# Performance work log

Hardware: AMD Instinct MI355X
Metric: run time of the kernel (lower is better)

The kernel has to match this reference:

```python
import jax, jax.numpy as jnp
import numpy as np

EMBED = 1024
HEADS = 16
HEAD_DIM = EMBED // HEADS
FFN = 4096
BSZ = 2
CHUNK = 128
NCHUNK = 16
REG_LEN = CHUNK * NCHUNK   # 2048
SUM_LEN = NCHUNK           # 1 summary token per chunk
NEG = -1e9


def _layer_norm(x, g, b, eps=1e-5):
    mu = x.mean(-1, keepdims=True)
    var = ((x - mu) ** 2).mean(-1, keepdims=True)
    return (x - mu) * jax.lax.rsqrt(var + eps) * g + b


def _build_mask(reg_chunk_ranges, sum_len, reg_len):
    # True = attention allowed. Museformer hierarchical scheme:
    #   rr: reg token attends reg tokens of its OWN chunk, causally
    #   rs: reg token attends summary tokens of STRICTLY EARLIER chunks
    #   sr: summary token of chunk c attends reg tokens of chunk c
    #   ss: causal among summary tokens
    bsz = reg_chunk_ranges.shape[0]
    starts = reg_chunk_ranges[:, :, 0]                       # [B, C]
    t = jnp.arange(reg_len)
    chunk_id = (t[None, :, None] >= starts[:, None, :]).sum(-1) - 1   # [B, R]
    sum_chunk = jnp.arange(sum_len)                          # [S]
    rr = (chunk_id[:, :, None] == chunk_id[:, None, :]) & (t[None, :, None] >= t[None, None, :])
    rs = sum_chunk[None, None, :] < chunk_id[:, :, None]     # [B, R, S]
    sr = chunk_id[:, None, :] == sum_chunk[None, :, None]    # [B, S, R]
    ss = jnp.broadcast_to(sum_chunk[:, None] >= sum_chunk[None, :], (bsz, sum_len, sum_len))
    top = jnp.concatenate([ss, sr], axis=2)
    bot = jnp.concatenate([rs, rr], axis=2)
    return jnp.concatenate([top, bot], axis=1)               # [B, S+R, S+R]


def _forward(x, w_q, w_k, w_v, w_o,
             ln_sa_sum_g, ln_sa_sum_b, ln_sa_reg_g, ln_sa_reg_b,
             sum_fc1_w, sum_fc1_b, sum_fc2_w, sum_fc2_b,
             reg_fc1_w, reg_fc1_b, reg_fc2_w, reg_fc2_b,
             ln_f_sum_g, ln_f_sum_b, ln_f_reg_g, ln_f_reg_b,
             reg_chunk_ranges, sum_len, reg_len):
    bsz, total, d = x.shape
    # --- self-attention block (pre-norm, separate LN for sum/reg parts) ---
    hs = _layer_norm(x[:, :sum_len], ln_sa_sum_g, ln_sa_sum_b)
    hr = _layer_norm(x[:, sum_len:], ln_sa_reg_g, ln_sa_reg_b)
    h = jnp.concatenate([hs, hr], axis=1)
    q = (h @ w_q.T).reshape(bsz, total, HEADS, HEAD_DIM)
    k = (h @ w_k.T).reshape(bsz, total, HEADS, HEAD_DIM)
    v = (h @ w_v.T).reshape(bsz, total, HEADS, HEAD_DIM)
    scores = jnp.einsum('bqhd,bkhd->bhqk', q, k) * (HEAD_DIM ** -0.5)
    mask = _build_mask(reg_chunk_ranges, sum_len, reg_len)   # [B, T, T] bool
    scores = jnp.where(mask[:, None], scores, NEG)
    attn = jax.nn.softmax(scores, axis=-1)
    ctx = jnp.einsum('bhqk,bkhd->bqhd', attn, v).reshape(bsz, total, d)
    x = x + ctx @ w_o.T
    # --- FFN block (pre-norm, separate LN/FFN for sum/reg parts) ---
    fs = _layer_norm(x[:, :sum_len], ln_f_sum_g, ln_f_sum_b)
    fs = jax.nn.relu(fs @ sum_fc1_w.T + sum_fc1_b) @ sum_fc2_w.T + sum_fc2_b
    fr = _layer_norm(x[:, sum_len:], ln_f_reg_g, ln_f_reg_b)
    fr = jax.nn.relu(fr @ reg_fc1_w.T + reg_fc1_b) @ reg_fc2_w.T + reg_fc2_b
    return x + jnp.concatenate([fs, fr], axis=1)


def setup_inputs() -> dict:
    key = jax.random.key(0)
    ks = jax.random.split(key, 12)
    s = 0.02
    total = SUM_LEN + REG_LEN
    starts = (np.arange(NCHUNK) * CHUNK).astype(np.int32)
    ranges = np.stack([starts, starts + CHUNK], axis=-1)     # [C, 2]
    reg_chunk_ranges = jnp.asarray(np.broadcast_to(ranges, (BSZ, NCHUNK, 2)).copy())
    d = dict(
        x=jax.random.normal(ks[0], (BSZ, total, EMBED), jnp.float32),
        w_q=jax.random.normal(ks[1], (EMBED, EMBED), jnp.float32) * s,
        w_k=jax.random.normal(ks[2], (EMBED, EMBED), jnp.float32) * s,
        w_v=jax.random.normal(ks[3], (EMBED, EMBED), jnp.float32) * s,
        w_o=jax.random.normal(ks[4], (EMBED, EMBED), jnp.float32) * s,
        ln_sa_sum_g=jnp.ones((EMBED,)), ln_sa_sum_b=jnp.zeros((EMBED,)),
        ln_sa_reg_g=jnp.ones((EMBED,)), ln_sa_reg_b=jnp.zeros((EMBED,)),
        sum_fc1_w=jax.random.normal(ks[5], (FFN, EMBED), jnp.float32) * s,
        sum_fc1_b=jnp.zeros((FFN,)),
        sum_fc2_w=jax.random.normal(ks[6], (EMBED, FFN), jnp.float32) * s,
        sum_fc2_b=jnp.zeros((EMBED,)),
        reg_fc1_w=jax.random.normal(ks[7], (FFN, EMBED), jnp.float32) * s,
        reg_fc1_b=jnp.zeros((FFN,)),
        reg_fc2_w=jax.random.normal(ks[8], (EMBED, FFN), jnp.float32) * s,
        reg_fc2_b=jnp.zeros((EMBED,)),
        ln_f_sum_g=jnp.ones((EMBED,)), ln_f_sum_b=jnp.zeros((EMBED,)),
        ln_f_reg_g=jnp.ones((EMBED,)), ln_f_reg_b=jnp.zeros((EMBED,)),
        reg_chunk_ranges=reg_chunk_ranges,
        sum_len=SUM_LEN,
        reg_len=REG_LEN,
    )
    return d


def reference(x, w_q, w_k, w_v, w_o,
              ln_sa_sum_g, ln_sa_sum_b, ln_sa_reg_g, ln_sa_reg_b,
              sum_fc1_w, sum_fc1_b, sum_fc2_w, sum_fc2_b,
              reg_fc1_w, reg_fc1_b, reg_fc2_w, reg_fc2_b,
              ln_f_sum_g, ln_f_sum_b, ln_f_reg_g, ln_f_reg_b,
              reg_chunk_ranges, sum_len, reg_len):
    return _forward(x, w_q, w_k, w_v, w_o,
                    ln_sa_sum_g, ln_sa_sum_b, ln_sa_reg_g, ln_sa_reg_b,
                    sum_fc1_w, sum_fc1_b, sum_fc2_w, sum_fc2_b,
                    reg_fc1_w, reg_fc1_b, reg_fc2_w, reg_fc2_b,
                    ln_f_sum_g, ln_f_sum_b, ln_f_reg_g, ln_f_reg_b,
                    reg_chunk_ranges, sum_len, reg_len)
```

## Files before the change

kernel.cpp:

```cpp
#include <hip/hip_runtime.h>
#include <stdint.h>

typedef __attribute__((ext_vector_type(8))) short short8;
typedef __attribute__((ext_vector_type(4))) float f32x4;

__device__ __forceinline__ float bf2f(short s) {
    union { unsigned u; float f; } c;
    c.u = ((unsigned)(unsigned short)s) << 16;
    return c.f;
}
__device__ __forceinline__ short f2bf(float f) {
    union { float f; unsigned u; } c; c.f = f;
    unsigned u = c.u + 0x7fffu + ((c.u >> 16) & 1u);
    return (short)(u >> 16);
}
__device__ __forceinline__ void gll16(const short* g, short* l) {
    __builtin_amdgcn_global_load_lds(
        (const __attribute__((address_space(1))) unsigned int*)g,
        (__attribute__((address_space(3))) unsigned int*)l, 16, 0, 0);
}

__global__ __launch_bounds__(256) void cvt_w(
    const float* __restrict__ wq, const float* __restrict__ wk,
    const float* __restrict__ wv, const float* __restrict__ wo,
    const float* __restrict__ f1s, const float* __restrict__ f2s,
    const float* __restrict__ f1r, const float* __restrict__ f2r,
    short* __restrict__ dst)
{
    size_t i = ((size_t)blockIdx.x * 256 + threadIdx.x) * 4;
    const float* src; size_t off;
    if (i < 4194304) {
        int seg = (int)(i >> 20);
        src = seg == 0 ? wq : seg == 1 ? wk : seg == 2 ? wv : wo;
        off = i & 1048575;
    } else {
        size_t ii = i - 4194304;
        int seg = (int)(ii >> 22);
        src = seg == 0 ? f1s : seg == 1 ? f2s : seg == 2 ? f1r : f2r;
        off = ii & 4194303;
    }
    float4 v = *(const float4*)(src + off);
    short4 o;
    o.x = f2bf(v.x); o.y = f2bf(v.y); o.z = f2bf(v.z); o.w = f2bf(v.w);
    *(short4*)(dst + i) = o;
}

template<int PHASE>
__global__ __launch_bounds__(256) void ln_k(
    const float* __restrict__ xin, const float* __restrict__ P, float* __restrict__ x1out,
    const float* __restrict__ g_sum, const float* __restrict__ b_sum,
    const float* __restrict__ g_reg, const float* __restrict__ b_reg,
    short* __restrict__ out_all, short* __restrict__ out_s, short* __restrict__ out_r)
{
    int row = blockIdx.x;
    int b = row / 2064, t = row - b * 2064;
    int tid = threadIdx.x;
    int c = tid * 4;
    size_t base = (size_t)row * 1024 + c;
    float4 v = *(const float4*)(xin + base);
    if (PHASE == 1) {
        float4 p0 = *(const float4*)(P + base);
        float4 p1 = *(const float4*)(P + base + 4227072);
        v.x += p0.x + p1.x; v.y += p0.y + p1.y;
        v.z += p0.z + p1.z; v.w += p0.w + p1.w;
        *(float4*)(x1out + base) = v;
    }
    float s = v.x + v.y + v.z + v.w;
#pragma unroll
    for (int off = 1; off < 64; off <<= 1) s += __shfl_xor(s, off);
    __shared__ float red[8];
    if ((tid & 63) == 0) red[tid >> 6] = s;
    __syncthreads();
    float mu = (red[0] + red[1] + red[2] + red[3]) * (1.0f / 1024.0f);
    float a0 = v.x - mu, a1 = v.y - mu, a2 = v.z - mu, a3 = v.w - mu;
    float qq = a0 * a0 + a1 * a1 + a2 * a2 + a3 * a3;
#pragma unroll
    for (int off = 1; off < 64; off <<= 1) qq += __shfl_xor(qq, off);
    if ((tid & 63) == 0) red[4 + (tid >> 6)] = qq;
    __syncthreads();
    float var = (red[4] + red[5] + red[6] + red[7]) * (1.0f / 1024.0f);
    float rs = rsqrtf(var + 1e-5f);
    const float* g  = (t < 16) ? g_sum : g_reg;
    const float* be = (t < 16) ? b_sum : b_reg;
    short4 o;
    o.x = f2bf(a0 * rs * g[c]     + be[c]);
    o.y = f2bf(a1 * rs * g[c + 1] + be[c + 1]);
    o.z = f2bf(a2 * rs * g[c + 2] + be[c + 2]);
    o.w = f2bf(a3 * rs * g[c + 3] + be[c + 3]);
    short* dst;
    if (PHASE == 0) dst = out_all + (size_t)row * 1024;
    else dst = (t < 16) ? (out_s + ((size_t)b * 16 + t) * 1024)
                        : (out_r + ((size_t)b * 2048 + (t - 16)) * 1024);
    *(short4*)(dst + c) = o;
}

template<int MODE>
__global__ __launch_bounds__(256) void gemm_bt(
    const short* __restrict__ A, int M, int K, int klen,
    const short* __restrict__ B0, const short* __restrict__ B1, const short* __restrict__ B2,
    const float* __restrict__ bias,
    void* __restrict__ o0, void* __restrict__ o1, void* __restrict__ o2, int seg)
{
    const int tid = threadIdx.x;
    const int w = tid >> 6, l = tid & 63;
    const int lr = l & 15, lh = l >> 4;
    const int m0 = blockIdx.x * 128;
    int ntile = blockIdx.y, nsel = 0;
    const short* B = B0;
    if (MODE == 0) { nsel = ntile >> 3; ntile &= 7; B = nsel == 0 ? B0 : (nsel == 1 ? B1 : B2); }
    const int n0 = ntile * 128;
    const int wr = (w >> 1) * 64, wc = (w & 1) * 64;
    const int kbase = blockIdx.z * klen;

    __shared__ __align__(16) short As[3 * 4096];
    __shared__ __align__(16) short Bs[3 * 4096];

    const int srow = w * 32 + (l >> 2);
    const int scol = (((l & 3) ^ ((l >> 3) & 3))) * 8;
    int ar0 = m0 + srow;      if (ar0 > M - 1) ar0 = M - 1;
    int ar1 = m0 + srow + 16; if (ar1 > M - 1) ar1 = M - 1;
    const short* ga0 = A + (size_t)ar0 * K + scol + kbase;
    const short* ga1 = A + (size_t)ar1 * K + scol + kbase;
    const short* gb0 = B + (size_t)(n0 + srow) * K + scol + kbase;
    const short* gb1 = B + (size_t)(n0 + srow + 16) * K + scol + kbase;
    const int lofs = (w * 32) * 32;

    const int cbrd = (lh ^ ((lr >> 1) & 3)) * 8;

    f32x4 acc[4][4];
#pragma unroll
    for (int m = 0; m < 4; ++m)
#pragma unroll
        for (int n = 0; n < 4; ++n) acc[m][n] = (f32x4){0.f, 0.f, 0.f, 0.f};

    auto STAGE = [&](int j, int s) {
        const int k0 = j * 32;
        short* a = As + s * 4096 + lofs;
        short* b = Bs + s * 4096 + lofs;
        gll16(ga0 + k0, a);
        gll16(ga1 + k0, a + 512);
        gll16(gb0 + k0, b);
        gll16(gb1 + k0, b + 512);
    };

    const int nk = klen >> 5;
    STAGE(0, 0);
    STAGE(1, 1);

    int sc = 0;
    for (int t = 0; t < nk; ++t) {
        if (t < nk - 1) asm volatile("s_waitcnt vmcnt(4)" ::: "memory");
        else            asm volatile("s_waitcnt vmcnt(0)" ::: "memory");
        __builtin_amdgcn_s_barrier();
        if (t + 2 < nk) {
            int sp = sc == 0 ? 2 : sc - 1;
            STAGE(t + 2, sp);
        }
        const int cur = sc * 4096;
        short8 af[4], bfr[4];
#pragma unroll
        for (int m = 0; m < 4; ++m)
            af[m] = *(const short8*)(As + cur + (wr + m * 16 + lr) * 32 + cbrd);
#pragma unroll
        for (int n = 0; n < 4; ++n)
            bfr[n] = *(const short8*)(Bs + cur + (wc + n * 16 + lr) * 32 + cbrd);
#pragma unroll
        for (int m = 0; m < 4; ++m)
#pragma unroll
            for (int n = 0; n < 4; ++n)
                acc[m][n] = __builtin_amdgcn_mfma_f32_16x16x32_bf16(af[m], bfr[n], acc[m][n], 0, 0, 0);
        sc = sc == 2 ? 0 : sc + 1;
    }

#pragma unroll
    for (int m = 0; m < 4; ++m) {
#pragma unroll
        for (int n = 0; n < 4; ++n) {
            int gc = n0 + wc + n * 16 + lr;
#pragma unroll
            for (int j = 0; j < 4; ++j) {
                int gr = m0 + wr + m * 16 + lh * 4 + j;
                if (gr >= M) continue;
                float val = acc[m][n][j];
                if (MODE == 0) {
                    short* o = (short*)(nsel == 0 ? o0 : (nsel == 1 ? o1 : o2));
                    o[(size_t)gr * 1024 + gc] = f2bf(val);
                } else if (MODE == 1) {
                    float* P = (float*)o0 + (size_t)blockIdx.z * (size_t)seg;
                    P[(size_t)gr * 1024 + gc] = val;
                } else {
                    val += bias[gc];
                    val = val > 0.f ? val : 0.f;
                    ((short*)o0)[(size_t)gr * 4096 + gc] = f2bf(val);
                }
            }
        }
    }
}

__global__ __launch_bounds__(256) void reduce_f2reg(
    const float* __restrict__ x1, const float* __restrict__ P,
    const float* __restrict__ bias, float* __restrict__ out)
{
    size_t i = ((size_t)blockIdx.x * 256 + threadIdx.x) * 4;
    int gr = (int)(i >> 10), c = (int)(i & 1023);
    size_t g = (size_t)((gr >> 11) * 2064 + 16 + (gr & 2047)) * 1024 + c;
    float4 p0 = *(const float4*)(P + i);
    float4 p1 = *(const float4*)(P + i + 4194304);
    float4 r  = *(const float4*)(x1 + g);
    float4 bb = *(const float4*)(bias + c);
    float4 o;
    o.x = r.x + p0.x + p1.x + bb.x; o.y = r.y + p0.y + p1.y + bb.y;
    o.z = r.z + p0.z + p1.z + bb.z; o.w = r.w + p0.w + p1.w + bb.w;
    *(float4*)(out + g) = o;
}

__global__ __launch_bounds__(256) void reduce_f2sum(
    const float* __restrict__ x1, const float* __restrict__ P,
    const float* __restrict__ bias, float* __restrict__ out)
{
    int i = (blockIdx.x * 256 + threadIdx.x) * 4;
    int gr = i >> 10, c = i & 1023;
    size_t g = (size_t)((gr >> 4) * 2064 + (gr & 15)) * 1024 + c;
    float4 r  = *(const float4*)(x1 + g);
    float4 bb = *(const float4*)(bias + c);
    float ox = r.x + bb.x, oy = r.y + bb.y, oz = r.z + bb.z, ow = r.w + bb.w;
#pragma unroll
    for (int s = 0; s < 16; ++s) {
        float4 p = *(const float4*)(P + s * 32768 + i);
        ox += p.x; oy += p.y; oz += p.z; ow += p.w;
    }
    float4 o; o.x = ox; o.y = oy; o.z = oz; o.w = ow;
    *(float4*)(out + g) = o;
}

__global__ __launch_bounds__(256) void attn_reg(
    const short* __restrict__ q, const short* __restrict__ k,
    const short* __restrict__ v, short* __restrict__ ctx)
{
    __shared__ __align__(16) short Pl[128 * 168];
    __shared__ __align__(16) short Vt[64 * 168];
    short* Kl = Pl;

    const int tid = threadIdx.x;
    const int w = tid >> 6, l = tid & 63, lr = l & 15, lh = l >> 4;
    const int c = blockIdx.x, h = blockIdx.y, b = blockIdx.z;
    const int hc = h * 64;
    const size_t rowq0 = (size_t)b * 2064 + 16 + (size_t)c * 128;

    for (int ch = tid; ch < 1152; ch += 256) {
        int row = ch >> 3, kk = (ch & 7) << 3;
        size_t grow = (row < 16) ? ((size_t)b * 2064 + row) : (rowq0 + row - 16);
        *(int4*)(Kl + row * 72 + kk) = *(const int4*)(k + grow * 1024 + hc + kk);
    }
    for (int ch = tid; ch < 1152; ch += 256) {
        int j = ch % 144, db = ch / 144;
        size_t grow = (j < 16) ? ((size_t)b * 2064 + j) : (rowq0 + j - 16);
        short8 dv = *(const short8*)(v + grow * 1024 + hc + db * 8);
#pragma unroll
        for (int i = 0; i < 8; ++i) Vt[(db * 8 + i) * 168 + j] = dv[i];
    }
    for (int idx = tid; idx < 1024; idx += 256) {
        int d = idx >> 4, jj = 144 + (idx & 15);
        Vt[d * 168 + jj] = 0;
    }
    __syncthreads();

    short8 qf[2][2];
#pragma unroll
    for (int m = 0; m < 2; ++m) {
        size_t grow = rowq0 + w * 32 + m * 16 + lr;
#pragma unroll
        for (int ks = 0; ks < 2; ++ks)
            qf[m][ks] = *(const short8*)(q + grow * 1024 + hc + ks * 32 + lh * 8);
    }

    f32x4 s[2][9];
#pragma unroll
    for (int m = 0; m < 2; ++m)
#pragma unroll
        for (int n = 0; n < 9; ++n) s[m][n] = (f32x4){0.f, 0.f, 0.f, 0.f};
#pragma unroll
    for (int n = 0; n < 9; ++n) {
        const short* kr = Kl + (n * 16 + lr) * 72;
        short8 k0 = *(const short8*)(kr + lh * 8);
        short8 k1 = *(const short8*)(kr + 32 + lh * 8);
        s[0][n] = __builtin_amdgcn_mfma_f32_16x16x32_bf16(qf[0][0], k0, s[0][n], 0, 0, 0);
        s[0][n] = __builtin_amdgcn_mfma_f32_16x16x32_bf16(qf[0][1], k1, s[0][n], 0, 0, 0);
        s[1][n] = __builtin_amdgcn_mfma_f32_16x16x32_bf16(qf[1][0], k0, s[1][n], 0, 0, 0);
        s[1][n] = __builtin_amdgcn_mfma_f32_16x16x32_bf16(qf[1][1], k1, s[1][n], 0, 0, 0);
    }

    float inv_[2][4];
#pragma unroll
    for (int m = 0; m < 2; ++m) {
#pragma unroll
        for (int j = 0; j < 4; ++j) {
            int p = w * 32 + m * 16 + lh * 4 + j;
            float best = -1e30f;
            float e[9];
#pragma unroll
            for (int n = 0; n < 9; ++n) {
                int kk = n * 16 + lr;
                bool vis = (kk < 16) ? (kk < c) : (kk - 16 <= p);
                float val = vis ? s[m][n][j] * 0.125f : -1e30f;
                e[n] = val;
                best = fmaxf(best, val);
            }
#pragma unroll
            for (int off = 1; off < 16; off <<= 1) best = fmaxf(best, __shfl_xor(best, off));
            float sm = 0.f;
#pragma unroll
            for (int n = 0; n < 9; ++n) {
                float ex = __expf(e[n] - best);
                s[m][n][j] = ex;
                sm += ex;
            }
#pragma unroll
            for (int off = 1; off < 16; off <<= 1) sm += __shfl_xor(sm, off);
            inv_[m][j] = 1.0f / sm;
        }
    }

    __syncthreads();
#pragma unroll
    for (int m = 0; m < 2; ++m)
#pragma unroll
        for (int n = 0; n < 9; ++n)
#pragma unroll
            for (int j = 0; j < 4; ++j)
                Pl[(w * 32 + m * 16 + lh * 4 + j) * 168 + n * 16 + lr] = f2bf(s[m][n][j]);
    for (int idx = l; idx < 512; idx += 64) {
        int rr = idx >> 4, kkp = 144 + (idx & 15);
        Pl[(w * 32 + rr) * 168 + kkp] = 0;
    }
    __syncthreads();

    f32x4 dacc[2][4];
#pragma unroll
    for (int m = 0; m < 2; ++m)
#pragma unroll
        for (int n = 0; n < 4; ++n) dacc[m][n] = (f32x4){0.f, 0.f, 0.f, 0.f};
#pragma unroll
    for (int ks = 0; ks < 5; ++ks) {
        int kk0 = ks * 32;
        short8 pa[2];
#pragma unroll
        for (int m = 0; m < 2; ++m)
            pa[m] = *(const short8*)(Pl + (w * 32 + m * 16 + lr) * 168 + kk0 + lh * 8);
#pragma unroll
        for (int n = 0; n < 4; ++n) {
            short8 vb = *(const short8*)(Vt + (n * 16 + lr) * 168 + kk0 + lh * 8);
            dacc[0][n] = __builtin_amdgcn_mfma_f32_16x16x32_bf16(pa[0], vb, dacc[0][n], 0, 0, 0);
            dacc[1][n] = __builtin_amdgcn_mfma_f32_16x16x32_bf16(pa[1], vb, dacc[1][n], 0, 0, 0);
        }
    }

#pragma unroll
    for (int m = 0; m < 2; ++m)
#pragma unroll
        for (int n = 0; n < 4; ++n)
#pragma unroll
            for (int j = 0; j < 4; ++j) {
                int p = w * 32 + m * 16 + lh * 4 + j;
                ctx[(rowq0 + p) * 1024 + hc + n * 16 + lr] = f2bf(dacc[m][n][j] * inv_[m][j]);
            }
}

__global__ __launch_bounds__(64) void attn_sum(
    const short* __restrict__ q, const short* __restrict__ k,
    const short* __restrict__ v, short* __restrict__ ctx)
{
    int idx = blockIdx.x;
    int b = idx >> 8, h = (idx >> 4) & 15, s = idx & 15;
    int l = threadIdx.x;
    int hc = h * 64;
    size_t qrow = (size_t)b * 2064 + s;
    __shared__ float qv[64];
    __shared__ float pp[192];
    qv[l] = bf2f(q[qrow * 1024 + hc + l]);
    __syncthreads();
    float sc[3];
#pragma unroll
    for (int i = 0; i < 3; ++i) {
        int j = l + i * 64;
        float t = -1e30f;
        if (j < 144 && (j >= 16 || j <= s)) {
            size_t kr = (j < 16) ? ((size_t)b * 2064 + j)
                                 : ((size_t)b * 2064 + 16 + (size_t)s * 128 + (j - 16));
            const short* kp = k + kr * 1024 + hc;
            float acc = 0.f;
            for (int d = 0; d < 64; ++d) acc += qv[d] * bf2f(kp[d]);
            t = acc * 0.125f;
        }
        sc[i] = t;
    }
    float mx = fmaxf(sc[0], fmaxf(sc[1], sc[2]));
#pragma unroll
    for (int off = 1; off < 64; off <<= 1) mx = fmaxf(mx, __shfl_xor(mx, off));
    float sm = 0.f;
#pragma unroll
    for (int i = 0; i < 3; ++i) {
        float ex = (sc[i] > -1e29f) ? __expf(sc[i] - mx) : 0.f;
        pp[l + i * 64] = ex;
        sm += ex;
    }
#pragma unroll
    for (int off = 1; off < 64; off <<= 1) sm += __shfl_xor(sm, off);
    __syncthreads();
    float invs = 1.0f / sm;
    float acc = 0.f;
    for (int j = 0; j < 144; ++j) {
        float pj = pp[j];
        size_t vr = (j < 16) ? ((size_t)b * 2064 + j)
                             : ((size_t)b * 2064 + 16 + (size_t)s * 128 + (j - 16));
        acc += pj * bf2f(v[vr * 1024 + hc + l]);
    }
    ctx[qrow * 1024 + hc + l] = f2bf(acc * invs);
}

extern "C" void kernel_launch(void* const* d_in, const int* in_sizes, int n_in,
                              void* d_out, int out_size, void* d_ws, size_t ws_size,
                              hipStream_t stream) {
    const float* x    = (const float*)d_in[0];
    const float* wq   = (const float*)d_in[1];
    const float* wk   = (const float*)d_in[2];
    const float* wv   = (const float*)d_in[3];
    const float* wo   = (const float*)d_in[4];
    const float* lsg  = (const float*)d_in[5];
    const float* lsb  = (const float*)d_in[6];
    const float* lrg  = (const float*)d_in[7];
    const float* lrb  = (const float*)d_in[8];
    const float* sf1w = (const float*)d_in[9];
    const float* sf1b = (const float*)d_in[10];
    const float* sf2w = (const float*)d_in[11];
    const float* sf2b = (const float*)d_in[12];
    const float* rf1w = (const float*)d_in[13];
    const float* rf1b = (const float*)d_in[14];
    const float* rf2w = (const float*)d_in[15];
    const float* rf2b = (const float*)d_in[16];
    const float* fsg  = (const float*)d_in[17];
    const float* fsb  = (const float*)d_in[18];
    const float* frg  = (const float*)d_in[19];
    const float* frb  = (const float*)d_in[20];
    float* out = (float*)d_out;

    char* ws = (char*)d_ws;
    short* wbf   = (short*)ws;
    short* wq_b  = wbf;
    short* wk_b  = wbf + 1048576;
    short* wv_b  = wbf + 2097152;
    short* wo_b  = wbf + 3145728;
    short* f1s_b = wbf + 4194304;
    short* f2s_b = wbf + 8388608;
    short* f1r_b = wbf + 12582912;
    short* f2r_b = wbf + 16777216;
    short* h_all = (short*)(ws + 41943040);
    short* qb   = (short*)(ws + 50397184);
    short* kb   = qb + 4227072;
    short* vb   = kb + 4227072;
    short* ctxb = vb + 4227072;
    float* Pwo = (float*)(ws + 41943040);
    float* x1 = (float*)(ws + 84213760);
    short* h2_reg = (short*)ws;
    short* h2_sum = (short*)(ws + 75759616);
    short* f1_reg = (short*)(ws + 41943040);
    short* f1_sum = (short*)(ws + 75825152);
    float* Psum = (float*)(ws + 8388608);
    float* Pf2 = (float*)ws;

    cvt_w<<<20480, 256, 0, stream>>>(wq, wk, wv, wo, sf1w, sf2w, rf1w, rf2w, wbf);
    ln_k<0><<<4128, 256, 0, stream>>>(x, nullptr, nullptr, lsg, lsb, lrg, lrb,
                                      h_all, nullptr, nullptr);
    gemm_bt<0><<<dim3(33, 24, 1), 256, 0, stream>>>(h_all, 4128, 1024, 1024,
        wq_b, wk_b, wv_b, nullptr, qb, kb, vb, 0);
    attn_reg<<<dim3(16, 16, 2), 256, 0, stream>>>(qb, kb, vb, ctxb);
    attn_sum<<<512, 64, 0, stream>>>(qb, kb, vb, ctxb);
    gemm_bt<1><<<dim3(33, 8, 2), 256, 0, stream>>>(ctxb, 4128, 1024, 512,
        wo_b, nullptr, nullptr, nullptr, Pwo, nullptr, nullptr, 4227072);
    ln_k<1><<<4128, 256, 0, stream>>>(x, Pwo, x1, fsg, fsb, frg, frb,
                                      nullptr, h2_sum, h2_reg);
    gemm_bt<2><<<dim3(32, 32, 1), 256, 0, stream>>>(h2_reg, 4096, 1024, 1024,
        f1r_b, nullptr, nullptr, rf1b, f1_reg, nullptr, nullptr, 0);
    gemm_bt<2><<<dim3(1, 32, 1), 256, 0, stream>>>(h2_sum, 32, 1024, 1024,
        f1s_b, nullptr, nullptr, sf1b, f1_sum, nullptr, nullptr, 0);
    gemm_bt<1><<<dim3(1, 8, 16), 256, 0, stream>>>(f1_sum, 32, 4096, 256,
        f2s_b, nullptr, nullptr, nullptr, Psum, nullptr, nullptr, 32768);
    reduce_f2sum<<<32, 256, 0, stream>>>(x1, Psum, sf2b, out);
    gemm_bt<1><<<dim3(32, 8, 2), 256, 0, stream>>>(f1_reg, 4096, 4096, 2048,
        f2r_b, nullptr, nullptr, nullptr, Pf2, nullptr, nullptr, 4194304);
    reduce_f2reg<<<4096, 256, 0, stream>>>(x1, Pf2, rf2b, out);
}
```

Measured before the change: 305.3 us.

## Use double-buffered GEMM pipeline, 4-way split-K with bf16 partials

The GEMM main loop goes from a 3-stage LDS ring with vmcnt-based waits to a 2-stage double buffer with a full __syncthreads each iteration. This cuts LDS use, which may raise occupancy. The output-projection and FFN2 GEMMs now split K four ways instead of two, which doubles the grid, and they write bf16 partials instead of fp32 to reduce partial-sum traffic. The downstream LN and reduce kernels sum four bf16 partials, which costs accuracy, and the simpler pipeline exposes more global-load latency.

Result: no change. 310.4 us (+1.7%).

```diff
diff --git a/kernel.cpp b/kernel.cpp
--- a/kernel.cpp
+++ b/kernel.cpp
@@ -47,7 +47,7 @@
 
 template<int PHASE>
 __global__ __launch_bounds__(256) void ln_k(
-    const float* __restrict__ xin, const float* __restrict__ P, float* __restrict__ x1out,
+    const float* __restrict__ xin, const short* __restrict__ Pw, float* __restrict__ x1out,
     const float* __restrict__ g_sum, const float* __restrict__ b_sum,
     const float* __restrict__ g_reg, const float* __restrict__ b_reg,
     short* __restrict__ out_all, short* __restrict__ out_s, short* __restrict__ out_r)
@@ -59,10 +59,12 @@
     size_t base = (size_t)row * 1024 + c;
     float4 v = *(const float4*)(xin + base);
     if (PHASE == 1) {
-        float4 p0 = *(const float4*)(P + base);
-        float4 p1 = *(const float4*)(P + base + 4227072);
-        v.x += p0.x + p1.x; v.y += p0.y + p1.y;
-        v.z += p0.z + p1.z; v.w += p0.w + p1.w;
+#pragma unroll
+        for (int z = 0; z < 4; ++z) {
+            short4 p = *(const short4*)(Pw + (size_t)z * 4227072 + base);
+            v.x += bf2f(p.x); v.y += bf2f(p.y);
+            v.z += bf2f(p.z); v.w += bf2f(p.w);
+        }
         *(float4*)(x1out + base) = v;
     }
     float s = v.x + v.y + v.z + v.w;
@@ -112,8 +114,8 @@
     const int wr = (w >> 1) * 64, wc = (w & 1) * 64;
     const int kbase = blockIdx.z * klen;
 
-    __shared__ __align__(16) short As[3 * 4096];
-    __shared__ __align__(16) short Bs[3 * 4096];
+    __shared__ __align__(16) short As[2 * 4096];
+    __shared__ __align__(16) short Bs[2 * 4096];
 
     const int srow = w * 32 + (l >> 2);
     const int scol = (((l & 3) ^ ((l >> 3) & 3))) * 8;
@@ -133,10 +135,10 @@
 #pragma unroll
         for (int n = 0; n < 4; ++n) acc[m][n] = (f32x4){0.f, 0.f, 0.f, 0.f};
 
-    auto STAGE = [&](int j, int s) {
+    auto STAGE = [&](int j, int buf) {
         const int k0 = j * 32;
-        short* a = As + s * 4096 + lofs;
-        short* b = Bs + s * 4096 + lofs;
+        short* a = As + buf * 4096 + lofs;
+        short* b = Bs + buf * 4096 + lofs;
         gll16(ga0 + k0, a);
         gll16(ga1 + k0, a + 512);
         gll16(gb0 + k0, b);
@@ -145,31 +147,23 @@
 
     const int nk = klen >> 5;
     STAGE(0, 0);
-    STAGE(1, 1);
-
-    int sc = 0;
     for (int t = 0; t < nk; ++t) {
-        if (t < nk - 1) asm volatile("s_waitcnt vmcnt(4)" ::: "memory");
-        else            asm volatile("s_waitcnt vmcnt(0)" ::: "memory");
-        __builtin_amdgcn_s_barrier();
-        if (t + 2 < nk) {
-            int sp = sc == 0 ? 2 : sc - 1;
-            STAGE(t + 2, sp);
-        }
-        const int cur = sc * 4096;
+        __syncthreads();
+        const int cur = (t & 1);
+        if (t + 1 < nk) STAGE(t + 1, cur ^ 1);
+        const int co = cur << 12;
         short8 af[4], bfr[4];
 #pragma unroll
         for (int m = 0; m < 4; ++m)
-            af[m] = *(const short8*)(As + cur + (wr + m * 16 + lr) * 32 + cbrd);
+            af[m] = *(const short8*)(As + co + (wr + m * 16 + lr) * 32 + cbrd);
 #pragma unroll
         for (int n = 0; n < 4; ++n)
-            bfr[n] = *(const short8*)(Bs + cur + (wc + n * 16 + lr) * 32 + cbrd);
+            bfr[n] = *(const short8*)(Bs + co + (wc + n * 16 + lr) * 32 + cbrd);
 #pragma unroll
         for (int m = 0; m < 4; ++m)
 #pragma unroll
             for (int n = 0; n < 4; ++n)
                 acc[m][n] = __builtin_amdgcn_mfma_f32_16x16x32_bf16(af[m], bfr[n], acc[m][n], 0, 0, 0);
-        sc = sc == 2 ? 0 : sc + 1;
     }
 
 #pragma unroll
@@ -188,10 +182,13 @@
                 } else if (MODE == 1) {
                     float* P = (float*)o0 + (size_t)blockIdx.z * (size_t)seg;
                     P[(size_t)gr * 1024 + gc] = val;
-                } else {
+                } else if (MODE == 2) {
                     val += bias[gc];
                     val = val > 0.f ? val : 0.f;
                     ((short*)o0)[(size_t)gr * 4096 + gc] = f2bf(val);
+                } else {
+                    short* P = (short*)o0 + (size_t)blockIdx.z * (size_t)seg;
+                    P[(size_t)gr * 1024 + gc] = f2bf(val);
                 }
             }
         }
@@ -199,19 +196,21 @@
 }
 
 __global__ __launch_bounds__(256) void reduce_f2reg(
-    const float* __restrict__ x1, const float* __restrict__ P,
+    const float* __restrict__ x1, const short* __restrict__ P,
     const float* __restrict__ bias, float* __restrict__ out)
 {
     size_t i = ((size_t)blockIdx.x * 256 + threadIdx.x) * 4;
     int gr = (int)(i >> 10), c = (int)(i & 1023);
     size_t g = (size_t)((gr >> 11) * 2064 + 16 + (gr & 2047)) * 1024 + c;
-    float4 p0 = *(const float4*)(P + i);
-    float4 p1 = *(const float4*)(P + i + 4194304);
     float4 r  = *(const float4*)(x1 + g);
     float4 bb = *(const float4*)(bias + c);
-    float4 o;
-    o.x = r.x + p0.x + p1.x + bb.x; o.y = r.y + p0.y + p1.y + bb.y;
-    o.z = r.z + p0.z + p1.z + bb.z; o.w = r.w + p0.w + p1.w + bb.w;
+    float ox = r.x + bb.x, oy = r.y + bb.y, oz = r.z + bb.z, ow = r.w + bb.w;
+#pragma unroll
+    for (int z = 0; z < 4; ++z) {
+        short4 p = *(const short4*)(P + (size_t)z * 4194304 + i);
+        ox += bf2f(p.x); oy += bf2f(p.y); oz += bf2f(p.z); ow += bf2f(p.w);
+    }
+    float4 o; o.x = ox; o.y = oy; o.z = oz; o.w = ow;
     *(float4*)(out + g) = o;
 }
 
@@ -460,14 +459,14 @@
     short* kb   = qb + 4227072;
     short* vb   = kb + 4227072;
     short* ctxb = vb + 4227072;
-    float* Pwo = (float*)(ws + 41943040);
+    short* Pwo = (short*)(ws + 41943040);
     float* x1 = (float*)(ws + 84213760);
     short* h2_reg = (short*)ws;
     short* h2_sum = (short*)(ws + 75759616);
     short* f1_reg = (short*)(ws + 41943040);
     short* f1_sum = (short*)(ws + 75825152);
     float* Psum = (float*)(ws + 8388608);
-    float* Pf2 = (float*)ws;
+    short* Pf2 = (short*)ws;
 
     cvt_w<<<20480, 256, 0, stream>>>(wq, wk, wv, wo, sf1w, sf2w, rf1w, rf2w, wbf);
     ln_k<0><<<4128, 256, 0, stream>>>(x, nullptr, nullptr, lsg, lsb, lrg, lrb,
@@ -476,7 +475,7 @@
         wq_b, wk_b, wv_b, nullptr, qb, kb, vb, 0);
     attn_reg<<<dim3(16, 16, 2), 256, 0, stream>>>(qb, kb, vb, ctxb);
     attn_sum<<<512, 64, 0, stream>>>(qb, kb, vb, ctxb);
-    gemm_bt<1><<<dim3(33, 8, 2), 256, 0, stream>>>(ctxb, 4128, 1024, 512,
+    gemm_bt<3><<<dim3(33, 8, 4), 256, 0, stream>>>(ctxb, 4128, 1024, 256,
         wo_b, nullptr, nullptr, nullptr, Pwo, nullptr, nullptr, 4227072);
     ln_k<1><<<4128, 256, 0, stream>>>(x, Pwo, x1, fsg, fsb, frg, frb,
                                       nullptr, h2_sum, h2_reg);
@@ -487,7 +486,7 @@
     gemm_bt<1><<<dim3(1, 8, 16), 256, 0, stream>>>(f1_sum, 32, 4096, 256,
         f2s_b, nullptr, nullptr, nullptr, Psum, nullptr, nullptr, 32768);
     reduce_f2sum<<<32, 256, 0, stream>>>(x1, Psum, sf2b, out);
-    gemm_bt<1><<<dim3(32, 8, 2), 256, 0, stream>>>(f1_reg, 4096, 4096, 2048,
+    gemm_bt<3><<<dim3(32, 8, 4), 256, 0, stream>>>(f1_reg, 4096, 4096, 1024,
         f2r_b, nullptr, nullptr, nullptr, Pf2, nullptr, nullptr, 4194304);
     reduce_f2reg<<<4096, 256, 0, stream>>>(x1, Pf2, rf2b, out);
 }
```
